# Kernel optimization log

Measured on AMD Instinct MI355X. Metric: run time of the kernel, lower is better.

The kernel has to match this reference:

```python
import jax, jax.numpy as jnp
import numpy as np

B, N, M, H = 32, 1024, 128, 2  # batch, memory slots, word size, read heads
EPS = 1e-8


def setup_inputs() -> dict:
    key = jax.random.key(0)
    ks = jax.random.split(key, 6)
    return {
        "read_keys": jax.random.normal(ks[0], (B, H, M), jnp.float32),
        "read_strengths": jax.random.uniform(ks[1], (B, H), jnp.float32),
        "read_mode": jax.random.uniform(ks[2], (B, H, 3), jnp.float32),
        "W_old": jax.random.uniform(ks[3], (B, N), jnp.float32),
        "L": jax.random.uniform(ks[4], (B, N, N), jnp.float32),
        "memory": jax.random.normal(ks[5], (B, N, M), jnp.float32),
        "head_no": 0,
    }


def reference(read_keys, read_strengths, read_mode, W_old, L, memory, head_no):
    # Select this head's parameters
    k = read_keys[:, head_no, :]                      # [B, M]
    beta = read_strengths[:, head_no][:, None]        # [B, 1]
    rm = read_mode[:, head_no, :]                     # [B, 3] (backward, content, forward)

    # Temporal link transitions: f = L @ w_old, b = L^T @ w_old
    f = jnp.einsum('bij,bj->bi', L, W_old)            # [B, N]
    b = jnp.einsum('bji,bj->bi', L, W_old)            # [B, N]

    # Content-based addressing: softmax(beta * cosine_similarity(k, memory))
    sim = jnp.einsum('bnm,bm->bn', memory, k)         # [B, N]
    denom = (jnp.linalg.norm(memory, axis=-1)
             * jnp.linalg.norm(k, axis=-1, keepdims=True)) + EPS
    C = jax.nn.softmax(beta * sim / denom, axis=-1)   # [B, N]

    # Read-mode weighted combination
    W = rm[:, 0:1] * b + rm[:, 1:2] * C + rm[:, 2:3] * f  # [B, N]

    # Memory read
    mem_content = jnp.einsum('bn,bnm->bm', W, memory)     # [B, M]
    return (W, mem_content)
```

## Files before the change

kernel.cpp:

```cpp
#include <hip/hip_runtime.h>
#include <math.h>

#define EPS 1e-8f

constexpr int B = 32, N = 1024, M = 128, H = 2;

constexpr int ROWS_A   = 16;
constexpr int CHUNKS_A = N / ROWS_A;
constexpr int NBLK_A   = B * CHUNKS_A;
constexpr int ROWS_B   = 64;
constexpr int NBLK_B   = B * (N / ROWS_B);
constexpr int ROWS_C   = 64;
constexpr int CHUNKS_C = N / ROWS_C;

__global__ __launch_bounds__(256) void k1(const float* __restrict__ L,
                                          const float* __restrict__ Wold,
                                          const float* __restrict__ mem,
                                          const float* __restrict__ keys,
                                          const float* __restrict__ strengths,
                                          const int* __restrict__ head,
                                          float* __restrict__ f,
                                          float* __restrict__ bpart,
                                          float* __restrict__ e) {
    int bid  = blockIdx.x;
    int t    = threadIdx.x;
    int lane = t & 63, wave = t >> 6;

    if (bid < NBLK_A) {
        __shared__ float sw[N];
        __shared__ float lds_b[4][N];

        int b     = bid / CHUNKS_A;
        int chunk = bid % CHUNKS_A;

        reinterpret_cast<float4*>(sw)[t] =
            reinterpret_cast<const float4*>(Wold + (size_t)b * N)[t];
        __syncthreads();

        float4 wreg[4];
        float4 bacc[4];
#pragma unroll
        for (int s = 0; s < 4; ++s) {
            wreg[s] = reinterpret_cast<float4*>(sw)[lane + 64 * s];
            bacc[s] = make_float4(0.f, 0.f, 0.f, 0.f);
        }

        const float* Lb = L + (size_t)b * N * N;
        int r0 = chunk * ROWS_A;
        for (int r = wave; r < ROWS_A; r += 4) {
            int i = r0 + r;
            const float4* row = reinterpret_cast<const float4*>(Lb + (size_t)i * N);
            float wi = sw[i];
            float p  = 0.f;
#pragma unroll
            for (int s = 0; s < 4; ++s) {
                float4 v = row[lane + 64 * s];
                p += v.x * wreg[s].x + v.y * wreg[s].y + v.z * wreg[s].z + v.w * wreg[s].w;
                bacc[s].x += v.x * wi;
                bacc[s].y += v.y * wi;
                bacc[s].z += v.z * wi;
                bacc[s].w += v.w * wi;
            }
#pragma unroll
            for (int off = 32; off; off >>= 1) p += __shfl_down(p, off, 64);
            if (lane == 0) f[(size_t)b * N + i] = p;
        }

#pragma unroll
        for (int s = 0; s < 4; ++s)
            reinterpret_cast<float4*>(lds_b[wave])[lane + 64 * s] = bacc[s];
        __syncthreads();

        float4 s0 = reinterpret_cast<float4*>(lds_b[0])[t];
        float4 s1 = reinterpret_cast<float4*>(lds_b[1])[t];
        float4 s2 = reinterpret_cast<float4*>(lds_b[2])[t];
        float4 s3 = reinterpret_cast<float4*>(lds_b[3])[t];
        float4 o;
        o.x = s0.x + s1.x + s2.x + s3.x;
        o.y = s0.y + s1.y + s2.y + s3.y;
        o.z = s0.z + s1.z + s2.z + s3.z;
        o.w = s0.w + s1.w + s2.w + s3.w;
        reinterpret_cast<float4*>(bpart + ((size_t)b * CHUNKS_A + chunk) * N)[t] = o;
    } else {
        int id    = bid - NBLK_A;
        int b     = id / (N / ROWS_B);
        int chunk = id % (N / ROWS_B);
        int half  = lane >> 5;
        int l32   = lane & 31;
        int h     = head[0];

        float4 kv = reinterpret_cast<const float4*>(keys + ((size_t)b * H + h) * M)[l32];
        float  sk = kv.x * kv.x + kv.y * kv.y + kv.z * kv.z + kv.w * kv.w;
#pragma unroll
        for (int off = 16; off; off >>= 1) sk += __shfl_xor(sk, off, 64);
        float norm_k = sqrtf(sk);
        float beta   = strengths[(size_t)b * H + h];

        int r0 = chunk * ROWS_B;
#pragma unroll
        for (int rr = 0; rr < ROWS_B / 8; ++rr) {
            int n = r0 + rr * 8 + wave * 2 + half;
            float4 mv = reinterpret_cast<const float4*>(mem + ((size_t)b * N + n) * M)[l32];
            float dot = mv.x * kv.x + mv.y * kv.y + mv.z * kv.z + mv.w * kv.w;
            float sm  = mv.x * mv.x + mv.y * mv.y + mv.z * mv.z + mv.w * mv.w;
#pragma unroll
            for (int off = 16; off; off >>= 1) {
                dot += __shfl_xor(dot, off, 64);
                sm  += __shfl_xor(sm, off, 64);
            }
            if (l32 == 0) {
                float denom = sqrtf(sm) * norm_k + EPS;
                e[(size_t)b * N + n] = expf(beta * dot / denom);
            }
        }
    }
}

__global__ __launch_bounds__(256) void k2(const float* __restrict__ mem,
                                          const float* __restrict__ bpart,
                                          const float* __restrict__ f,
                                          const float* __restrict__ e,
                                          const float* __restrict__ mode,
                                          const int* __restrict__ head,
                                          float* __restrict__ U,
                                          float* __restrict__ mcU,
                                          float* __restrict__ mcE,
                                          float* __restrict__ epart) {
    int bid   = blockIdx.x;
    int b     = bid / CHUNKS_C;
    int chunk = bid % CHUNKS_C;
    int t     = threadIdx.x;
    int r0    = chunk * ROWS_C;

    __shared__ float bp[4][ROWS_C];
    __shared__ float su[ROWS_C], se[ROWS_C];
    __shared__ float4 lU[8][32];
    __shared__ float4 lE[8][32];

    int n_ = t & 63, cg_ = t >> 6;
    float s = 0.f;
    for (int c = cg_; c < CHUNKS_A; c += 4)
        s += bpart[((size_t)b * CHUNKS_A + c) * N + r0 + n_];
    bp[cg_][n_] = s;
    __syncthreads();

    int h = head[0];
    const float* rm = mode + ((size_t)b * H + h) * 3;
    if (t < ROWS_C) {
        float bsum = bp[0][t] + bp[1][t] + bp[2][t] + bp[3][t];
        float u = rm[0] * bsum + rm[2] * f[(size_t)b * N + r0 + t];
        su[t] = u;
        U[(size_t)b * N + r0 + t] = u;
        se[t] = e[(size_t)b * N + r0 + t];
    }
    __syncthreads();

    int cg = t & 31, rg = t >> 5;
    float4 aU = make_float4(0.f, 0.f, 0.f, 0.f);
    float4 aE = make_float4(0.f, 0.f, 0.f, 0.f);
#pragma unroll
    for (int rr = 0; rr < ROWS_C / 8; ++rr) {
        int r = rg + rr * 8;
        float4 v = reinterpret_cast<const float4*>(mem + ((size_t)b * N + r0 + r) * M)[cg];
        float uu = su[r], ee = se[r];
        aU.x += uu * v.x; aU.y += uu * v.y; aU.z += uu * v.z; aU.w += uu * v.w;
        aE.x += ee * v.x; aE.y += ee * v.y; aE.z += ee * v.z; aE.w += ee * v.w;
    }
    lU[rg][cg] = aU;
    lE[rg][cg] = aE;
    __syncthreads();

    if (t < 32) {
        float4 oU = make_float4(0.f, 0.f, 0.f, 0.f);
        float4 oE = make_float4(0.f, 0.f, 0.f, 0.f);
#pragma unroll
        for (int g = 0; g < 8; ++g) {
            float4 vU = lU[g][t], vE = lE[g][t];
            oU.x += vU.x; oU.y += vU.y; oU.z += vU.z; oU.w += vU.w;
            oE.x += vE.x; oE.y += vE.y; oE.z += vE.z; oE.w += vE.w;
        }
        reinterpret_cast<float4*>(mcU + ((size_t)b * CHUNKS_C + chunk) * M)[t] = oU;
        reinterpret_cast<float4*>(mcE + ((size_t)b * CHUNKS_C + chunk) * M)[t] = oE;
    } else if (t >= 64 && t < 128) {
        float val = se[t - 64];
#pragma unroll
        for (int off = 32; off; off >>= 1) val += __shfl_down(val, off, 64);
        if (t == 64) epart[(size_t)b * CHUNKS_C + chunk] = val;
    }
}

__global__ __launch_bounds__(256) void k3(const float* __restrict__ U,
                                          const float* __restrict__ e,
                                          const float* __restrict__ mcU,
                                          const float* __restrict__ mcE,
                                          const float* __restrict__ epart,
                                          const float* __restrict__ mode,
                                          const int* __restrict__ head,
                                          float* __restrict__ outW,
                                          float* __restrict__ outMC) {
    int b = blockIdx.x;
    int t = threadIdx.x;
    int h = head[0];
    float rm1 = mode[((size_t)b * H + h) * 3 + 1];

    float S = 0.f;
#pragma unroll
    for (int c = 0; c < CHUNKS_C; ++c) S += epart[(size_t)b * CHUNKS_C + c];
    float coef = rm1 / S;

#pragma unroll
    for (int q = 0; q < 4; ++q) {
        int n = t + 256 * q;
        outW[(size_t)b * N + n] = U[(size_t)b * N + n] + coef * e[(size_t)b * N + n];
    }
    if (t < M) {
        float sU = 0.f, sE = 0.f;
#pragma unroll
        for (int c = 0; c < CHUNKS_C; ++c) {
            sU += mcU[((size_t)b * CHUNKS_C + c) * M + t];
            sE += mcE[((size_t)b * CHUNKS_C + c) * M + t];
        }
        outMC[(size_t)b * M + t] = sU + coef * sE;
    }
}

extern "C" void kernel_launch(void* const* d_in, const int* in_sizes, int n_in,
                              void* d_out, int out_size, void* d_ws, size_t ws_size,
                              hipStream_t stream) {
    const float* read_keys      = (const float*)d_in[0];
    const float* read_strengths = (const float*)d_in[1];
    const float* read_mode      = (const float*)d_in[2];
    const float* W_old          = (const float*)d_in[3];
    const float* L              = (const float*)d_in[4];
    const float* memory         = (const float*)d_in[5];
    const int*   head_no        = (const int*)d_in[6];

    float* out_W  = (float*)d_out;
    float* out_mc = out_W + (size_t)B * N;

    float* ws    = (float*)d_ws;
    float* f     = ws;
    float* bpart = f + (size_t)B * N;
    float* e     = bpart + (size_t)B * CHUNKS_A * N;
    float* Ubuf  = e + (size_t)B * N;
    float* mcU   = Ubuf + (size_t)B * N;
    float* mcE   = mcU + (size_t)B * CHUNKS_C * M;
    float* epart = mcE + (size_t)B * CHUNKS_C * M;

    k1<<<NBLK_A + NBLK_B, 256, 0, stream>>>(L, W_old, memory, read_keys,
                                            read_strengths, head_no, f, bpart, e);
    k2<<<B * CHUNKS_C, 256, 0, stream>>>(memory, bpart, f, e, read_mode, head_no,
                                         Ubuf, mcU, mcE, epart);
    k3<<<B, 256, 0, stream>>>(Ubuf, e, mcU, mcE, epart, read_mode, head_no,
                              out_W, out_mc);
}
```

Before: 41.27 us.

## Merge content-addressing into link blocks, fuse final kernel via last-block counter

The separate content-similarity blocks are folded into every link-matrix block, so each block also handles its 16 memory rows. The third kernel is removed: the last k2 block per batch, found with an atomic counter and threadfence, does the softmax normalization and final combination. L rows are now read with nontemporal loads. This trades one kernel launch for a memset, an atomic and a tail-block serial step.

```diff
diff --git a/kernel.cpp b/kernel.cpp
--- a/kernel.cpp
+++ b/kernel.cpp
@@ -8,10 +8,10 @@
 constexpr int ROWS_A   = 16;
 constexpr int CHUNKS_A = N / ROWS_A;
 constexpr int NBLK_A   = B * CHUNKS_A;
-constexpr int ROWS_B   = 64;
-constexpr int NBLK_B   = B * (N / ROWS_B);
 constexpr int ROWS_C   = 64;
 constexpr int CHUNKS_C = N / ROWS_C;
+
+typedef float floatx4 __attribute__((ext_vector_type(4)));
 
 __global__ __launch_bounds__(256) void k1(const float* __restrict__ L,
                                           const float* __restrict__ Wold,
@@ -22,84 +22,60 @@
                                           float* __restrict__ f,
                                           float* __restrict__ bpart,
                                           float* __restrict__ e) {
-    int bid  = blockIdx.x;
-    int t    = threadIdx.x;
-    int lane = t & 63, wave = t >> 6;
-
-    if (bid < NBLK_A) {
-        __shared__ float sw[N];
-        __shared__ float lds_b[4][N];
-
-        int b     = bid / CHUNKS_A;
-        int chunk = bid % CHUNKS_A;
-
-        reinterpret_cast<float4*>(sw)[t] =
-            reinterpret_cast<const float4*>(Wold + (size_t)b * N)[t];
-        __syncthreads();
-
-        float4 wreg[4];
-        float4 bacc[4];
+    int bid   = blockIdx.x;
+    int t     = threadIdx.x;
+    int lane  = t & 63, wave = t >> 6;
+    int b     = bid / CHUNKS_A;
+    int chunk = bid % CHUNKS_A;
+    int r0    = chunk * ROWS_A;
+
+    __shared__ float sw[N];
+    __shared__ float lds_b[4][N];
+
+    reinterpret_cast<float4*>(sw)[t] =
+        reinterpret_cast<const float4*>(Wold + (size_t)b * N)[t];
+    __syncthreads();
+
+    float4 wreg[4];
+    float4 bacc[4];
+#pragma unroll
+    for (int s = 0; s < 4; ++s) {
+        wreg[s] = reinterpret_cast<float4*>(sw)[lane + 64 * s];
+        bacc[s] = make_float4(0.f, 0.f, 0.f, 0.f);
+    }
+
+    const float* Lb = L + (size_t)b * N * N;
+    for (int r = wave; r < ROWS_A; r += 4) {
+        int i = r0 + r;
+        const floatx4* row = reinterpret_cast<const floatx4*>(Lb + (size_t)i * N);
+        float wi = sw[i];
+        float p  = 0.f;
 #pragma unroll
         for (int s = 0; s < 4; ++s) {
-            wreg[s] = reinterpret_cast<float4*>(sw)[lane + 64 * s];
-            bacc[s] = make_float4(0.f, 0.f, 0.f, 0.f);
-        }
-
-        const float* Lb = L + (size_t)b * N * N;
-        int r0 = chunk * ROWS_A;
-        for (int r = wave; r < ROWS_A; r += 4) {
-            int i = r0 + r;
-            const float4* row = reinterpret_cast<const float4*>(Lb + (size_t)i * N);
-            float wi = sw[i];
-            float p  = 0.f;
-#pragma unroll
-            for (int s = 0; s < 4; ++s) {
-                float4 v = row[lane + 64 * s];
-                p += v.x * wreg[s].x + v.y * wreg[s].y + v.z * wreg[s].z + v.w * wreg[s].w;
-                bacc[s].x += v.x * wi;
-                bacc[s].y += v.y * wi;
-                bacc[s].z += v.z * wi;
-                bacc[s].w += v.w * wi;
-            }
-#pragma unroll
-            for (int off = 32; off; off >>= 1) p += __shfl_down(p, off, 64);
-            if (lane == 0) f[(size_t)b * N + i] = p;
-        }
-
-#pragma unroll
-        for (int s = 0; s < 4; ++s)
-            reinterpret_cast<float4*>(lds_b[wave])[lane + 64 * s] = bacc[s];
-        __syncthreads();
-
-        float4 s0 = reinterpret_cast<float4*>(lds_b[0])[t];
-        float4 s1 = reinterpret_cast<float4*>(lds_b[1])[t];
-        float4 s2 = reinterpret_cast<float4*>(lds_b[2])[t];
-        float4 s3 = reinterpret_cast<float4*>(lds_b[3])[t];
-        float4 o;
-        o.x = s0.x + s1.x + s2.x + s3.x;
-        o.y = s0.y + s1.y + s2.y + s3.y;
-        o.z = s0.z + s1.z + s2.z + s3.z;
-        o.w = s0.w + s1.w + s2.w + s3.w;
-        reinterpret_cast<float4*>(bpart + ((size_t)b * CHUNKS_A + chunk) * N)[t] = o;
-    } else {
-        int id    = bid - NBLK_A;
-        int b     = id / (N / ROWS_B);
-        int chunk = id % (N / ROWS_B);
-        int half  = lane >> 5;
-        int l32   = lane & 31;
-        int h     = head[0];
-
+            floatx4 v = __builtin_nontemporal_load(row + lane + 64 * s);
+            p += v.x * wreg[s].x + v.y * wreg[s].y + v.z * wreg[s].z + v.w * wreg[s].w;
+            bacc[s].x += v.x * wi;
+            bacc[s].y += v.y * wi;
+            bacc[s].z += v.z * wi;
+            bacc[s].w += v.w * wi;
+        }
+#pragma unroll
+        for (int off = 32; off; off >>= 1) p += __shfl_down(p, off, 64);
+        if (lane == 0) f[(size_t)b * N + i] = p;
+    }
+
+    {
+        int l32 = lane & 31, half = lane >> 5;
+        int h   = head[0];
         float4 kv = reinterpret_cast<const float4*>(keys + ((size_t)b * H + h) * M)[l32];
         float  sk = kv.x * kv.x + kv.y * kv.y + kv.z * kv.z + kv.w * kv.w;
 #pragma unroll
         for (int off = 16; off; off >>= 1) sk += __shfl_xor(sk, off, 64);
         float norm_k = sqrtf(sk);
         float beta   = strengths[(size_t)b * H + h];
-
-        int r0 = chunk * ROWS_B;
-#pragma unroll
-        for (int rr = 0; rr < ROWS_B / 8; ++rr) {
-            int n = r0 + rr * 8 + wave * 2 + half;
+#pragma unroll
+        for (int rr = 0; rr < ROWS_A / 8; ++rr) {
+            int n = r0 + wave * 4 + rr * 2 + half;
             float4 mv = reinterpret_cast<const float4*>(mem + ((size_t)b * N + n) * M)[l32];
             float dot = mv.x * kv.x + mv.y * kv.y + mv.z * kv.z + mv.w * kv.w;
             float sm  = mv.x * mv.x + mv.y * mv.y + mv.z * mv.z + mv.w * mv.w;
@@ -114,6 +90,22 @@
             }
         }
     }
+
+#pragma unroll
+    for (int s = 0; s < 4; ++s)
+        reinterpret_cast<float4*>(lds_b[wave])[lane + 64 * s] = bacc[s];
+    __syncthreads();
+
+    float4 s0 = reinterpret_cast<float4*>(lds_b[0])[t];
+    float4 s1 = reinterpret_cast<float4*>(lds_b[1])[t];
+    float4 s2 = reinterpret_cast<float4*>(lds_b[2])[t];
+    float4 s3 = reinterpret_cast<float4*>(lds_b[3])[t];
+    float4 o;
+    o.x = s0.x + s1.x + s2.x + s3.x;
+    o.y = s0.y + s1.y + s2.y + s3.y;
+    o.z = s0.z + s1.z + s2.z + s3.z;
+    o.w = s0.w + s1.w + s2.w + s3.w;
+    reinterpret_cast<float4*>(bpart + ((size_t)b * CHUNKS_A + chunk) * N)[t] = o;
 }
 
 __global__ __launch_bounds__(256) void k2(const float* __restrict__ mem,
@@ -125,7 +117,10 @@
                                           float* __restrict__ U,
                                           float* __restrict__ mcU,
                                           float* __restrict__ mcE,
-                                          float* __restrict__ epart) {
+                                          float* __restrict__ epart,
+                                          unsigned int* __restrict__ ctr,
+                                          float* __restrict__ outW,
+                                          float* __restrict__ outMC) {
     int bid   = blockIdx.x;
     int b     = bid / CHUNKS_C;
     int chunk = bid % CHUNKS_C;
@@ -136,6 +131,7 @@
     __shared__ float su[ROWS_C], se[ROWS_C];
     __shared__ float4 lU[8][32];
     __shared__ float4 lE[8][32];
+    __shared__ unsigned int sOld;
 
     int n_ = t & 63, cg_ = t >> 6;
     float s = 0.f;
@@ -187,40 +183,36 @@
         for (int off = 32; off; off >>= 1) val += __shfl_down(val, off, 64);
         if (t == 64) epart[(size_t)b * CHUNKS_C + chunk] = val;
     }
-}
-
-__global__ __launch_bounds__(256) void k3(const float* __restrict__ U,
-                                          const float* __restrict__ e,
-                                          const float* __restrict__ mcU,
-                                          const float* __restrict__ mcE,
-                                          const float* __restrict__ epart,
-                                          const float* __restrict__ mode,
-                                          const int* __restrict__ head,
-                                          float* __restrict__ outW,
-                                          float* __restrict__ outMC) {
-    int b = blockIdx.x;
-    int t = threadIdx.x;
-    int h = head[0];
-    float rm1 = mode[((size_t)b * H + h) * 3 + 1];
-
-    float S = 0.f;
-#pragma unroll
-    for (int c = 0; c < CHUNKS_C; ++c) S += epart[(size_t)b * CHUNKS_C + c];
-    float coef = rm1 / S;
-
-#pragma unroll
-    for (int q = 0; q < 4; ++q) {
-        int n = t + 256 * q;
-        outW[(size_t)b * N + n] = U[(size_t)b * N + n] + coef * e[(size_t)b * N + n];
-    }
-    if (t < M) {
-        float sU = 0.f, sE = 0.f;
-#pragma unroll
-        for (int c = 0; c < CHUNKS_C; ++c) {
-            sU += mcU[((size_t)b * CHUNKS_C + c) * M + t];
-            sE += mcE[((size_t)b * CHUNKS_C + c) * M + t];
-        }
-        outMC[(size_t)b * M + t] = sU + coef * sE;
+
+    __threadfence();
+    __syncthreads();
+    if (t == 0) sOld = atomicAdd(&ctr[b], 1u);
+    __syncthreads();
+    if (sOld == CHUNKS_C - 1) {
+        __threadfence();
+        float S = 0.f;
+#pragma unroll
+        for (int c = 0; c < CHUNKS_C; ++c) S += epart[(size_t)b * CHUNKS_C + c];
+        float coef = rm[1] / S;
+
+        float4 u  = reinterpret_cast<const float4*>(U + (size_t)b * N)[t];
+        float4 ev = reinterpret_cast<const float4*>(e + (size_t)b * N)[t];
+        float4 o;
+        o.x = u.x + coef * ev.x;
+        o.y = u.y + coef * ev.y;
+        o.z = u.z + coef * ev.z;
+        o.w = u.w + coef * ev.w;
+        reinterpret_cast<float4*>(outW + (size_t)b * N)[t] = o;
+
+        if (t < M) {
+            float sU = 0.f, sE = 0.f;
+#pragma unroll
+            for (int c = 0; c < CHUNKS_C; ++c) {
+                sU += mcU[((size_t)b * CHUNKS_C + c) * M + t];
+                sE += mcE[((size_t)b * CHUNKS_C + c) * M + t];
+            }
+            outMC[(size_t)b * M + t] = sU + coef * sE;
+        }
     }
 }
 
@@ -246,11 +238,11 @@
     float* mcU   = Ubuf + (size_t)B * N;
     float* mcE   = mcU + (size_t)B * CHUNKS_C * M;
     float* epart = mcE + (size_t)B * CHUNKS_C * M;
-
-    k1<<<NBLK_A + NBLK_B, 256, 0, stream>>>(L, W_old, memory, read_keys,
-                                            read_strengths, head_no, f, bpart, e);
+    unsigned int* ctr = (unsigned int*)(epart + (size_t)B * CHUNKS_C);
+
+    (void)hipMemsetAsync(ctr, 0, B * sizeof(unsigned int), stream);
+    k1<<<NBLK_A, 256, 0, stream>>>(L, W_old, memory, read_keys,
+                                   read_strengths, head_no, f, bpart, e);
     k2<<<B * CHUNKS_C, 256, 0, stream>>>(memory, bpart, f, e, read_mode, head_no,
-                                         Ubuf, mcU, mcE, epart);
-    k3<<<B, 256, 0, stream>>>(Ubuf, e, mcU, mcE, epart, read_mode, head_no,
-                              out_W, out_mc);
+                                         Ubuf, mcU, mcE, epart, ctr, out_W, out_mc);
 }
```

After: 94.95 us. 130% more time.
